# Kernel optimization log

Hardware: AMD Instinct MI355X
Metric: run time of the kernel (lower is better)

## Reference

```python
import jax, jax.numpy as jnp
import numpy as np

E, H, V, P, RAW = 512, 1024, 12000, 36, 2048
B, L = 128, 21

def setup_inputs() -> dict:
    key = jax.random.key(0)
    ks = jax.random.split(key, 16)
    n = lambda k, sh: (0.02 * jax.random.normal(k, sh)).astype(jnp.float32)
    z = lambda sh: jnp.zeros(sh, jnp.float32)
    return {
        "images_features": jax.random.normal(ks[0], (B, P, RAW), dtype=jnp.float32),
        "encoded_captions": jax.random.randint(ks[1], (B, L), 0, V),
        "caption_lengths": L,
        "W_img": n(ks[2], (RAW, H)), "b_img": z((H,)),
        "W_glob": n(ks[3], (H, E)), "b_glob": z((E,)),
        "W_ih1": n(ks[4], (2 * E + H, 4 * H)), "W_hh1": n(ks[5], (H, 4 * H)),
        "b_ih1": z((4 * H,)), "b_hh1": z((4 * H,)),
        "Wx_gate": n(ks[6], (2 * E + H, H)), "bx_gate": z((H,)),
        "Wh_gate": n(ks[7], (H, H)), "bh_gate": z((H,)),
        "W_ih2": n(ks[8], (2 * H, 4 * H)), "W_hh2": n(ks[9], (H, 4 * H)),
        "b_ih2": z((4 * H,)), "b_hh2": z((4 * H,)),
        "Wv": n(ks[10], (H, P)), "bv": z((P,)),
        "Ws": n(ks[11], (H, P)), "bs": z((P,)),
        "Wg": n(ks[12], (H, P)),
        "wh": n(ks[13], (P,)),
        "emb": n(ks[14], (V, E)),
        "W_fc": n(ks[15], (H, V)), "b_fc": z((V,)),
    }

def _lstm(x, h, c, W_ih, W_hh, b_ih, b_hh):
    # torch LSTMCell gate order: i, f, g, o
    g = x @ W_ih + b_ih + h @ W_hh + b_hh
    i, f, gg, o = jnp.split(g, 4, axis=-1)
    c_new = jax.nn.sigmoid(f) * c + jax.nn.sigmoid(i) * jnp.tanh(gg)
    h_new = jax.nn.sigmoid(o) * jnp.tanh(c_new)
    return h_new, c_new

def reference(images_features, encoded_captions, caption_lengths, W_img, b_img,
              W_glob, b_glob, W_ih1, W_hh1, b_ih1, b_hh1, Wx_gate, bx_gate,
              Wh_gate, bh_gate, W_ih2, W_hh2, b_ih2, b_hh2, Wv, bv, Ws, bs,
              Wg, wh, emb, W_fc, b_fc):
    Bsz = images_features.shape[0]
    Hd = W_hh1.shape[0]
    T = int(caption_lengths) - 1
    Vfeat = jax.nn.relu(images_features @ W_img + b_img)            # (B,P,H)
    glob = jax.nn.relu(jnp.mean(Vfeat, axis=1) @ W_glob + b_glob)   # (B,E)
    img_proj = Vfeat @ Wv + bv                                      # (B,P,P) loop-invariant
    word_embs = emb[encoded_captions[:, :T]]                        # (B,T,E)

    def step(carry, we):
        h1, c1, h2, c2 = carry
        xt = jnp.concatenate([h2, glob, we], axis=-1)               # (B, H+2E)
        h1n, c1n = _lstm(xt, h1, c1, W_ih1, W_hh1, b_ih1, b_hh1)
        sen_gate = jax.nn.sigmoid(xt @ Wx_gate + bx_gate + h1 @ Wh_gate + bh_gate)
        st = sen_gate * jnp.tanh(c1n)                               # visual sentinel
        ht_proj = h1n @ Wg                                          # (B,P)
        z = jnp.tanh(img_proj + ht_proj[:, :, None]) @ wh           # (B,P)
        alpha = jax.nn.softmax(z, axis=1)                           # (B,P)
        context = jnp.einsum('bp,bph->bh', alpha, Vfeat)            # (B,H)
        att_vs = jnp.tanh(st @ Ws + bs + ht_proj) @ wh              # (B,)
        alpha_hat = jax.nn.softmax(jnp.concatenate([z, att_vs[:, None]], axis=1), axis=1)
        beta = alpha_hat[:, -1:]                                    # (B,1)
        c_hat = beta * st + (1.0 - beta) * context
        h2n, c2n = _lstm(jnp.concatenate([c_hat, h1n], axis=-1), h2, c2,
                         W_ih2, W_hh2, b_ih2, b_hh2)
        score = (c_hat + h2n) @ W_fc + b_fc                         # (B,V)
        return (h1n, c1n, h2n, c2n), (score, alpha, beta)

    zeros = jnp.zeros((Bsz, Hd), images_features.dtype)
    init = (zeros, zeros, zeros, zeros)
    _, (preds, alphas, betas) = jax.lax.scan(step, init, jnp.swapaxes(word_embs, 0, 1))
    return (jnp.swapaxes(preds, 0, 1),   # (B,T,V)
            jnp.swapaxes(alphas, 0, 1),  # (B,T,P)
            jnp.swapaxes(betas, 0, 1))   # (B,T,1)
```

## Files before the change

### kernel.cpp

```cpp
#include <hip/hip_runtime.h>
#include <hip/hip_bf16.h>
#include <math.h>

typedef __attribute__((ext_vector_type(4))) float f32x4;
typedef __attribute__((ext_vector_type(8))) short bf16x8;

constexpr int kB = 128, kT = 20, kH = 1024, kE = 512, kP = 36, kRaw = 2048, kV = 12000;
constexpr int kSlab1 = kB * 5120;
constexpr int kSlab2 = kB * 4096;

__device__ __forceinline__ float sigf(float x) { return 1.0f / (1.0f + expf(-x)); }

#define AS1C const __attribute__((address_space(1))) void*
#define AS3P __attribute__((address_space(3))) void*

constexpr int NZ1 = 2 * kB * kH / 4;
constexpr int NZ2 = 2 * kB * kH * 2 / 16;
constexpr int NCV = kB * kP * kRaw / 4;
constexpr int NPV = 64 * 1024 * 2 / 16;
constexpr int NPF = 32 * 1024 * 2 / 16;
constexpr int NPB = 5120;
constexpr int NGE = kB * kT * kE;

__global__ __launch_bounds__(256) void prep_small(
    float* c1z, uint4* h1z, const float* images, __hip_bfloat16* imagesb,
    uint4* wtv, uint4* wtfc_pad,
    const float* b_ih1, const float* b_hh1, const float* bx, const float* bh,
    const float* b_ih2, const float* b_hh2, float* bias_g1, float* bias_g2,
    const int* caps, const float* emb, __hip_bfloat16* wembb) {
  long idx = (long)blockIdx.x * 256 + threadIdx.x;
  if (idx < NZ1) { reinterpret_cast<float4*>(c1z)[idx] = make_float4(0, 0, 0, 0); return; }
  idx -= NZ1;
  if (idx < NZ2) { h1z[idx] = make_uint4(0, 0, 0, 0); return; }
  idx -= NZ2;
  if (idx < NCV) {
    float4 v = reinterpret_cast<const float4*>(images)[idx];
    __hip_bfloat16* d = imagesb + idx * 4;
    d[0] = __float2bfloat16(v.x); d[1] = __float2bfloat16(v.y);
    d[2] = __float2bfloat16(v.z); d[3] = __float2bfloat16(v.w);
    return;
  }
  idx -= NCV;
  if (idx < NPV) { wtv[idx] = make_uint4(0, 0, 0, 0); return; }
  idx -= NPV;
  if (idx < NPF) { wtfc_pad[idx] = make_uint4(0, 0, 0, 0); return; }
  idx -= NPF;
  if (idx < NPB) {
    int i = (int)idx;
    if (i < 4096) {
      bias_g1[i] = b_ih1[i] + b_hh1[i];
      bias_g2[i] = b_ih2[i] + b_hh2[i];
    } else {
      bias_g1[i] = bx[i - 4096] + bh[i - 4096];
    }
    return;
  }
  idx -= NPB;
  if (idx < NGE) {
    int e = (int)(idx % kE);
    int bt = (int)(idx / kE);
    int t = bt % kT;
    int b = bt / kT;
    int tok = caps[b * (kT + 1) + t];
    wembb[idx] = __float2bfloat16(emb[(size_t)tok * kE + e]);
  }
}

struct TJob {
  const float* src; __hip_bfloat16* dst;
  int ld_src, K, N, lddst, koff, noff, blk_off, nbx;
};
struct TAll { TJob job[12]; int njobs; int total_blocks; };

__global__ __launch_bounds__(256) void transpose_all(TAll ta) {
  __shared__ float t[32][33];
  int bid = blockIdx.x;
  int ji = 0;
  while (ji + 1 < ta.njobs && bid >= ta.job[ji + 1].blk_off) ++ji;
  const TJob& J = ta.job[ji];
  int lbid = bid - J.blk_off;
  int n0 = (lbid % J.nbx) * 32, k0 = (lbid / J.nbx) * 32;
  int tx = threadIdx.x & 31, ty = threadIdx.x >> 5;
  #pragma unroll
  for (int i = 0; i < 32; i += 8) {
    int k = k0 + ty + i, n = n0 + tx;
    t[ty + i][tx] = (k < J.K && n < J.N) ? J.src[(size_t)k * J.ld_src + n] : 0.0f;
  }
  __syncthreads();
  #pragma unroll
  for (int i = 0; i < 32; i += 8) {
    int n = n0 + ty + i, k = k0 + tx;
    if (n < J.N && k < J.K)
      J.dst[(size_t)(n + J.noff) * J.lddst + k + J.koff] = __float2bfloat16(t[tx][ty + i]);
  }
}

struct SegB { const __hip_bfloat16* A; int lda; int kstart; int kend; };
struct GemmBArgs {
  SegB seg[4]; int nseg;
  const __hip_bfloat16* WT; int ldk;
  const float* bias;
  float* C; __hip_bfloat16* C16; int ldc; int N; int Ktot; int act; int zstride;
};

__global__ __launch_bounds__(256) void gemm_bf16(GemmBArgs ga) {
  __shared__ char lds[65536];
  const int bm = blockIdx.y * 64;
  const int bn = blockIdx.x * 64;
  const int tid = threadIdx.x;
  const int lane = tid & 63;
  const int w = tid >> 6;
  const int wr = w >> 1, wc = w & 1;

  int rowS[4], scbS[4], dstS[4];
  #pragma unroll
  for (int j = 0; j < 4; ++j) {
    int off = ((j * 4 + w) * 64 + lane) * 16;
    int row = off >> 8, colb = off & 255;
    rowS[j] = row;
    scbS[j] = colb ^ ((row & 7) << 4);
    dstS[j] = (j * 4 + w) * 1024;
  }

  f32x4 acc[2][2] = {};
  const int nz = gridDim.z;
  const int nit = (ga.Ktot >> 7) / nz;
  const int it0 = blockIdx.z * nit;
  float* C = ga.C + (size_t)blockIdx.z * ga.zstride;

  auto stage = [&](int it, int buf) {
    const int k0 = it << 7;
    int si = 0;
    while (k0 >= ga.seg[si].kend) ++si;
    const __hip_bfloat16* Aseg = ga.seg[si].A;
    const int lda = ga.seg[si].lda;
    const int ks = k0 - ga.seg[si].kstart;
    char* baseA = lds + buf * 32768;
    char* baseB = baseA + 16384;
    #pragma unroll
    for (int j = 0; j < 4; ++j) {
      const __hip_bfloat16* sA = Aseg + (size_t)(bm + rowS[j]) * lda + ks + (scbS[j] >> 1);
      __builtin_amdgcn_global_load_lds((AS1C)sA, (AS3P)(baseA + dstS[j]), 16, 0, 0);
      const __hip_bfloat16* sB = ga.WT + (size_t)(bn + rowS[j]) * ga.ldk + k0 + (scbS[j] >> 1);
      __builtin_amdgcn_global_load_lds((AS1C)sB, (AS3P)(baseB + dstS[j]), 16, 0, 0);
    }
  };

  auto compute = [&](int buf) {
    const char* baseA = lds + buf * 32768;
    const char* baseB = baseA + 16384;
    #pragma unroll
    for (int kk = 0; kk < 4; ++kk) {
      bf16x8 a[2], b[2];
      #pragma unroll
      for (int f = 0; f < 2; ++f) {
        int row = wr * 32 + f * 16 + (lane & 15);
        int cb = kk * 64 + (lane >> 4) * 16;
        a[f] = *(const bf16x8*)(baseA + row * 256 + (cb ^ ((row & 7) << 4)));
        int nl = wc * 32 + f * 16 + (lane & 15);
        b[f] = *(const bf16x8*)(baseB + nl * 256 + (cb ^ ((nl & 7) << 4)));
      }
      #pragma unroll
      for (int fm = 0; fm < 2; ++fm)
        #pragma unroll
        for (int fn = 0; fn < 2; ++fn)
          acc[fm][fn] = __builtin_amdgcn_mfma_f32_16x16x32_bf16(a[fm], b[fn], acc[fm][fn], 0, 0, 0);
    }
  };

  stage(it0, 0);
  stage(it0 + 1, 1);
  asm volatile("s_waitcnt vmcnt(8)" ::: "memory");
  __builtin_amdgcn_s_barrier();
  int cur = 0;
  for (int i = 0; i < nit; ++i) {
    compute(cur);
    __builtin_amdgcn_s_barrier();
    if (i + 2 < nit) stage(it0 + i + 2, cur);
    if (i + 1 < nit) {
      if (i + 2 < nit) asm volatile("s_waitcnt vmcnt(8)" ::: "memory");
      else             asm volatile("s_waitcnt vmcnt(0)" ::: "memory");
      __builtin_amdgcn_s_barrier();
    }
    cur ^= 1;
  }

  #pragma unroll
  for (int fm = 0; fm < 2; ++fm) {
    int rbase = bm + wr * 32 + fm * 16 + (lane >> 4) * 4;
    #pragma unroll
    for (int fn = 0; fn < 2; ++fn) {
      int col = bn + wc * 32 + fn * 16 + (lane & 15);
      if (col >= ga.N) continue;
      float bv = ga.bias ? ga.bias[col] : 0.0f;
      #pragma unroll
      for (int j = 0; j < 4; ++j) {
        float v = acc[fm][fn][j] + bv;
        if (ga.act == 1) v = fmaxf(v, 0.0f);
        size_t off = (size_t)(rbase + j) * ga.ldc + col;
        if (ga.C) C[off] = v;
        if (ga.C16) ga.C16[off] = __float2bfloat16(v);
      }
    }
  }
}

struct G128Args {
  const __hip_bfloat16* A; int lda;
  const __hip_bfloat16* WT; int ldk;
  const float* bias;
  float* C; __hip_bfloat16* C16; int ldc; int N; int Ktot; int act; int cmap; int morder;
};

template <int BK>
__global__ __launch_bounds__(256) void gemm128(G128Args ga) {
  constexpr int RB = BK * 2;
  constexpr int TILEB = 128 * RB;
  constexpr int ROUNDS = TILEB / 4096;
  constexpr int SWZ = (RB == 256) ? 15 : (RB == 128 ? 7 : 3);
  __shared__ char lds[2 * 2 * TILEB];
  const int gx = gridDim.x;
  const int gy = gridDim.y;
  const int nwg = gx * gy;
  int bid = blockIdx.y * gx + blockIdx.x;
  int q = nwg >> 3, r = nwg & 7;
  int xc = bid & 7, yq = bid >> 3;
  int swz = (xc < r ? xc * (q + 1) : r * (q + 1) + (xc - r) * q) + yq;
  int bn, bm;
  if (ga.morder == 1) { bm = (swz % gy) * 128; bn = (swz / gy) * 128; }
  else                { bn = (swz % gx) * 128; bm = (swz / gx) * 128; }

  const int tid = threadIdx.x;
  const int lane = tid & 63;
  const int w = tid >> 6;
  const int wr = w >> 1, wc = w & 1;

  int rowS[ROUNDS], scbS[ROUNDS], dstS[ROUNDS];
  #pragma unroll
  for (int j = 0; j < ROUNDS; ++j) {
    int off = ((j * 4 + w) * 64 + lane) * 16;
    int row = off / RB, colb = off % RB;
    rowS[j] = row;
    scbS[j] = colb ^ ((row & SWZ) << 4);
    dstS[j] = off;
  }

  f32x4 acc[4][4] = {};
  const int nit = ga.Ktot / BK;

  auto stage = [&](int it, int buf) {
    const int k0 = it * BK;
    char* baseA = lds + buf * 2 * TILEB;
    char* baseB = baseA + TILEB;
    #pragma unroll
    for (int j = 0; j < ROUNDS; ++j) {
      const __hip_bfloat16* sA = ga.A + (size_t)(bm + rowS[j]) * ga.lda + k0 + (scbS[j] >> 1);
      __builtin_amdgcn_global_load_lds((AS1C)sA, (AS3P)(baseA + dstS[j]), 16, 0, 0);
      const __hip_bfloat16* sB = ga.WT + (size_t)(bn + rowS[j]) * ga.ldk + k0 + (scbS[j] >> 1);
      __builtin_amdgcn_global_load_lds((AS1C)sB, (AS3P)(baseB + dstS[j]), 16, 0, 0);
    }
  };

  auto compute = [&](int buf) {
    const char* baseA = lds + buf * 2 * TILEB;
    const char* baseB = baseA + TILEB;
    #pragma unroll
    for (int kk = 0; kk < BK / 32; ++kk) {
      bf16x8 a[4], b[4];
      int cb = kk * 64 + (lane >> 4) * 16;
      #pragma unroll
      for (int f = 0; f < 4; ++f) {
        int row = wr * 64 + f * 16 + (lane & 15);
        a[f] = *(const bf16x8*)(baseA + row * RB + (cb ^ ((row & SWZ) << 4)));
        int nl = wc * 64 + f * 16 + (lane & 15);
        b[f] = *(const bf16x8*)(baseB + nl * RB + (cb ^ ((nl & SWZ) << 4)));
      }
      #pragma unroll
      for (int fm = 0; fm < 4; ++fm)
        #pragma unroll
        for (int fn = 0; fn < 4; ++fn)
          acc[fm][fn] = __builtin_amdgcn_mfma_f32_16x16x32_bf16(a[fm], b[fn], acc[fm][fn], 0, 0, 0);
    }
  };

  auto wait_one_stage = [&]() {
    if constexpr (ROUNDS == 4) asm volatile("s_waitcnt vmcnt(8)" ::: "memory");
    else                       asm volatile("s_waitcnt vmcnt(4)" ::: "memory");
  };

  stage(0, 0);
  stage(1, 1);
  wait_one_stage();
  __builtin_amdgcn_s_barrier();
  int cur = 0;
  for (int i = 0; i < nit; ++i) {
    compute(cur);
    __builtin_amdgcn_s_barrier();
    if (i + 2 < nit) stage(i + 2, cur);
    if (i + 1 < nit) {
      if (i + 2 < nit) wait_one_stage();
      else             asm volatile("s_waitcnt vmcnt(0)" ::: "memory");
      __builtin_amdgcn_s_barrier();
    }
    cur ^= 1;
  }

  #pragma unroll
  for (int fm = 0; fm < 4; ++fm) {
    int rbase = bm + wr * 64 + fm * 16 + (lane >> 4) * 4;
    #pragma unroll
    for (int fn = 0; fn < 4; ++fn) {
      int col = bn + wc * 64 + fn * 16 + (lane & 15);
      if (col >= ga.N) continue;
      float bv = ga.bias ? ga.bias[col] : 0.0f;
      #pragma unroll
      for (int j = 0; j < 4; ++j) {
        float v = acc[fm][fn][j] + bv;
        if (ga.act == 1) v = fmaxf(v, 0.0f);
        int m = rbase + j;
        size_t off = ga.cmap == 1
            ? (size_t)(m & 127) * ga.ldc + (size_t)(m >> 7) * kV + col
            : (size_t)m * ga.ldc + col;
        if (ga.C) ga.C[off] = v;
        if (ga.C16) ga.C16[off] = __float2bfloat16(v);
      }
    }
  }
}

__global__ __launch_bounds__(256) void mean_p(const float* __restrict__ Vfeat,
                                              __hip_bfloat16* __restrict__ meanVb) {
  int idx = blockIdx.x * 256 + threadIdx.x;
  if (idx >= kB * kH) return;
  int b = idx >> 10, h = idx & 1023;
  float sm = 0.0f;
  for (int p = 0; p < kP; ++p) sm += Vfeat[((size_t)b * kP + p) * kH + h];
  meanVb[idx] = __float2bfloat16(sm * (1.0f / kP));
}

__global__ __launch_bounds__(256) void step1_fused(
    const float* __restrict__ g, const float* __restrict__ bias_g1,
    float* __restrict__ c1, __hip_bfloat16* __restrict__ h1b,
    const float* __restrict__ img_proj, const float* __restrict__ Vfeat,
    const float* __restrict__ Wg, const float* __restrict__ Ws,
    const float* __restrict__ bs, const float* __restrict__ wh,
    float* __restrict__ c_hat, __hip_bfloat16* __restrict__ c_hatb,
    float* __restrict__ out_alphas, float* __restrict__ out_betas, int t) {
  const int b = blockIdx.x;
  const int tid = threadIdx.x;
  const int lane = tid & 63;
  const int w = tid >> 6;
  __shared__ float sh_h1[kH];
  __shared__ float sh_st[kH];
  __shared__ float wsum[4][36];
  __shared__ float htp[36];
  __shared__ float stp[36];
  __shared__ float alpha[kP];
  __shared__ float sred[4];

  const float* gr0 = g + (size_t)b * 5120;
  const float* gr1 = gr0 + kSlab1;
  const float* gr2 = gr1 + kSlab1;
  #pragma unroll
  for (int i = 0; i < 4; ++i) {
    int h = tid + i * 256;
    float ig = sigf(gr0[h]           + gr1[h]           + gr2[h]           + bias_g1[h]);
    float fg = sigf(gr0[kH + h]      + gr1[kH + h]      + gr2[kH + h]      + bias_g1[kH + h]);
    float gg = tanhf(gr0[2 * kH + h] + gr1[2 * kH + h]  + gr2[2 * kH + h]  + bias_g1[2 * kH + h]);
    float og = sigf(gr0[3 * kH + h]  + gr1[3 * kH + h]  + gr2[3 * kH + h]  + bias_g1[3 * kH + h]);
    int idx = b * kH + h;
    float c = fg * c1[idx] + ig * gg;
    float tc = tanhf(c);
    float hn = og * tc;
    c1[idx] = c;
    h1b[idx] = __float2bfloat16(hn);
    sh_h1[h] = hn;
    sh_st[h] = sigf(gr0[4 * kH + h] + gr1[4 * kH + h] + gr2[4 * kH + h] + bias_g1[4 * kH + h]) * tc;
  }
  __syncthreads();

  #pragma unroll
  for (int pass = 0; pass < 2; ++pass) {
    const float* vec = pass == 0 ? sh_h1 : sh_st;
    const float* W = pass == 0 ? Wg : Ws;
    float pg[36];
    #pragma unroll
    for (int j = 0; j < 36; ++j) pg[j] = 0.0f;
    #pragma unroll
    for (int i = 0; i < 4; ++i) {
      int hh = tid + i * 256;
      float hv = vec[hh];
      const float4* wrow = reinterpret_cast<const float4*>(W + (size_t)hh * 36);
      #pragma unroll
      for (int r = 0; r < 9; ++r) {
        float4 wv = wrow[r];
        pg[4 * r + 0] = fmaf(hv, wv.x, pg[4 * r + 0]);
        pg[4 * r + 1] = fmaf(hv, wv.y, pg[4 * r + 1]);
        pg[4 * r + 2] = fmaf(hv, wv.z, pg[4 * r + 2]);
        pg[4 * r + 3] = fmaf(hv, wv.w, pg[4 * r + 3]);
      }
    }
    #pragma unroll
    for (int j = 0; j < 36; ++j) {
      float v = pg[j];
      #pragma unroll
      for (int off = 32; off > 0; off >>= 1) v += __shfl_down(v, off, 64);
      if (lane == 0) wsum[w][j] = v;
    }
    __syncthreads();
    if (tid < 36) {
      float s = wsum[0][tid] + wsum[1][tid] + wsum[2][tid] + wsum[3][tid];
      if (pass == 0) htp[tid] = s; else stp[tid] = s;
    }
    __syncthreads();
  }

  if (w == 0) {
    float zz_r = -3.0e38f;
    if (lane < kP) {
      const float* ip = img_proj + ((size_t)b * kP + lane) * kP;
      float acc = 0.0f;
      #pragma unroll
      for (int j = 0; j < kP; ++j) acc = fmaf(tanhf(ip[j] + htp[j]), wh[j], acc);
      zz_r = acc;
    }
    float m = zz_r;
    #pragma unroll
    for (int off = 32; off > 0; off >>= 1) m = fmaxf(m, __shfl_xor(m, off, 64));
    float e = (lane < kP) ? expf(zz_r - m) : 0.0f;
    float s = e;
    #pragma unroll
    for (int off = 32; off > 0; off >>= 1) s += __shfl_xor(s, off, 64);
    if (lane < kP) alpha[lane] = e / s;
    if (lane == 0) { sred[2] = m; sred[3] = s; }
  } else if (w == 1) {
    float tv = 0.0f;
    if (lane < kP) tv = tanhf(stp[lane] + bs[lane] + htp[lane]) * wh[lane];
    #pragma unroll
    for (int off = 32; off > 0; off >>= 1) tv += __shfl_xor(tv, off, 64);
    if (lane == 0) sred[0] = tv;
  }
  __syncthreads();
  if (tid == 0) {
    float av = sred[0], m = sred[2], s = sred[3];
    float m2 = fmaxf(m, av);
    float eb = expf(av - m2);
    float beta = eb / (s * expf(m - m2) + eb);
    sred[1] = beta;
    out_betas[b * kT + t] = beta;
  }
  __syncthreads();
  if (tid < kP) out_alphas[((size_t)b * kT + t) * kP + tid] = alpha[tid];
  const float beta = sred[1];
  #pragma unroll
  for (int i = 0; i < 4; ++i) {
    int h = tid + i * 256;
    float ctx = 0.0f;
    for (int p = 0; p < kP; ++p) ctx = fmaf(alpha[p], Vfeat[((size_t)b * kP + p) * kH + h], ctx);
    float v = beta * sh_st[h] + (1.0f - beta) * ctx;
    c_hat[(size_t)b * kH + h] = v;
    c_hatb[(size_t)b * kH + h] = __float2bfloat16(v);
  }
}

__global__ __launch_bounds__(256) void lstm2_elem(const float* __restrict__ g,
                                                  const float* __restrict__ bias_g2,
                                                  float* __restrict__ c2,
                                                  __hip_bfloat16* __restrict__ h2b,
                                                  const float* __restrict__ c_hat,
                                                  __hip_bfloat16* __restrict__ sbufb) {
  int idx = blockIdx.x * 256 + threadIdx.x;
  if (idx >= kB * kH) return;
  int b = idx >> 10, h = idx & 1023;
  const float* gr0 = g + (size_t)b * 4 * kH;
  const float* gr1 = gr0 + kSlab2;
  const float* gr2 = gr1 + kSlab2;
  float ig = sigf(gr0[h]           + gr1[h]           + gr2[h]           + bias_g2[h]);
  float fg = sigf(gr0[kH + h]      + gr1[kH + h]      + gr2[kH + h]      + bias_g2[kH + h]);
  float gg = tanhf(gr0[2 * kH + h] + gr1[2 * kH + h]  + gr2[2 * kH + h]  + bias_g2[2 * kH + h]);
  float og = sigf(gr0[3 * kH + h]  + gr1[3 * kH + h]  + gr2[3 * kH + h]  + bias_g2[3 * kH + h]);
  float c = fg * c2[idx] + ig * gg;
  float hn = og * tanhf(c);
  c2[idx] = c;
  h2b[idx] = __float2bfloat16(hn);
  sbufb[idx] = __float2bfloat16(c_hat[idx] + hn);
}

extern "C" void kernel_launch(void* const* d_in, const int* in_sizes, int n_in,
                              void* d_out, int out_size, void* d_ws, size_t ws_size,
                              hipStream_t stream) {
  const float* images  = (const float*)d_in[0];
  const int*   caps    = (const int*)d_in[1];
  const float* W_img   = (const float*)d_in[3];
  const float* b_img   = (const float*)d_in[4];
  const float* W_glob  = (const float*)d_in[5];
  const float* b_glob  = (const float*)d_in[6];
  const float* W_ih1   = (const float*)d_in[7];
  const float* W_hh1   = (const float*)d_in[8];
  const float* b_ih1   = (const float*)d_in[9];
  const float* b_hh1   = (const float*)d_in[10];
  const float* Wx_gate = (const float*)d_in[11];
  const float* bx_gate = (const float*)d_in[12];
  const float* Wh_gate = (const float*)d_in[13];
  const float* bh_gate = (const float*)d_in[14];
  const float* W_ih2   = (const float*)d_in[15];
  const float* W_hh2   = (const float*)d_in[16];
  const float* b_ih2   = (const float*)d_in[17];
  const float* b_hh2   = (const float*)d_in[18];
  const float* Wv      = (const float*)d_in[19];
  const float* bv      = (const float*)d_in[20];
  const float* Ws_     = (const float*)d_in[21];
  const float* bs_     = (const float*)d_in[22];
  const float* Wg      = (const float*)d_in[23];
  const float* wh      = (const float*)d_in[24];
  const float* emb     = (const float*)d_in[25];
  const float* W_fc    = (const float*)d_in[26];
  const float* b_fc    = (const float*)d_in[27];

  float* out = (float*)d_out;
  float* out_alphas = out + (size_t)kB * kT * kV;
  float* out_betas  = out_alphas + (size_t)kB * kT * kP;

  char* base = (char*)d_ws;
  auto alloc = [&](size_t bytes) {
    char* p = base;
    base += (bytes + 255) & ~(size_t)255;
    return p;
  };
  float*          Vfeat   = (float*)alloc((size_t)kB * kP * kH * 4);
  __hip_bfloat16* Vfeatb  = (__hip_bfloat16*)alloc((size_t)kB * kP * kH * 2);
  __hip_bfloat16* imagesb = (__hip_bfloat16*)alloc((size_t)kB * kP * kRaw * 2);
  __hip_bfloat16* WTg1    = (__hip_bfloat16*)alloc((size_t)5120 * 3072 * 2);
  __hip_bfloat16* WTg2    = (__hip_bfloat16*)alloc((size_t)4096 * 3072 * 2);
  __hip_bfloat16* WTfc    = (__hip_bfloat16*)alloc((size_t)12032 * 1024 * 2);
  __hip_bfloat16* WTimg   = (__hip_bfloat16*)alloc((size_t)1024 * 2048 * 2);
  __hip_bfloat16* WTglob  = (__hip_bfloat16*)alloc((size_t)512 * 1024 * 2);
  __hip_bfloat16* WTv     = (__hip_bfloat16*)alloc((size_t)64 * 1024 * 2);
  __hip_bfloat16* wembb   = (__hip_bfloat16*)alloc((size_t)kB * kT * kE * 2);
  float*          img_proj= (float*)alloc((size_t)kB * kP * kP * 4);
  __hip_bfloat16* globb   = (__hip_bfloat16*)alloc((size_t)kB * kE * 2);
  __hip_bfloat16* meanVb  = (__hip_bfloat16*)alloc((size_t)kB * kH * 2);
  float*          c1      = (float*)alloc((size_t)2 * kB * kH * 4);
  float*          c2      = c1 + kB * kH;
  __hip_bfloat16* h1b     = (__hip_bfloat16*)alloc((size_t)2 * kB * kH * 2);
  __hip_bfloat16* h2b     = h1b + kB * kH;
  float*          g1out   = (float*)alloc((size_t)3 * kB * 5120 * 4);
  float*          chat    = (float*)alloc((size_t)kB * kH * 4);
  __hip_bfloat16* chatb   = (__hip_bfloat16*)alloc((size_t)kB * kH * 2);
  __hip_bfloat16* sbufall = (__hip_bfloat16*)alloc((size_t)kT * kB * kH * 2);
  float*          bias_g1 = (float*)alloc(5120 * 4);
  float*          bias_g2 = (float*)alloc(4096 * 4);

  {
    long total = (long)NZ1 + NZ2 + NCV + NPV + NPF + NPB + NGE;
    int blocks = (int)((total + 255) / 256);
    prep_small<<<blocks, 256, 0, stream>>>(
        c1, (uint4*)h1b, images, imagesb, (uint4*)WTv,
        (uint4*)(WTfc + (size_t)12000 * 1024),
        b_ih1, b_hh1, bx_gate, bh_gate, b_ih2, b_hh2, bias_g1, bias_g2,
        caps, emb, wembb);
  }
  {
    TAll ta = {};
    int off = 0, j = 0;
    auto add = [&](const float* src, int ldsrc, int K, int N, __hip_bfloat16* dst,
                   int lddst, int koff, int noff) {
      int nbx = (N + 31) / 32, nby = (K + 31) / 32;
      ta.job[j] = {src, dst, ldsrc, K, N, lddst, koff, noff, off, nbx};
      off += nbx * nby;
      ++j;
    };
    add(W_img,   kH,     kRaw, kH,     WTimg,  kRaw, 0, 0);
    add(W_glob,  kE,     kH,   kE,     WTglob, kH,   0, 0);
    add(Wv,      kP,     kH,   kP,     WTv,    kH,   0, 0);
    add(W_ih1,   4 * kH, 2048, 4 * kH, WTg1,   3072, 0, 0);
    add(W_hh1,   4 * kH, 1024, 4 * kH, WTg1,   3072, 2048, 0);
    add(Wx_gate, kH,     2048, kH,     WTg1,   3072, 0, 4096);
    add(Wh_gate, kH,     1024, kH,     WTg1,   3072, 2048, 4096);
    add(W_ih2,   4 * kH, 2048, 4 * kH, WTg2,   3072, 0, 0);
    add(W_hh2,   4 * kH, 1024, 4 * kH, WTg2,   3072, 2048, 0);
    add(W_fc,    kV,     kH,   kV,     WTfc,   kH,   0, 0);
    ta.njobs = j;
    ta.total_blocks = off;
    transpose_all<<<off, 256, 0, stream>>>(ta);
  }

  {
    G128Args ga = {};
    ga.A = imagesb; ga.lda = kRaw; ga.WT = WTimg; ga.ldk = kRaw; ga.bias = b_img;
    ga.C = Vfeat; ga.C16 = Vfeatb; ga.ldc = kH; ga.N = kH; ga.Ktot = kRaw;
    ga.act = 1; ga.cmap = 0; ga.morder = 0;
    gemm128<64><<<dim3(kH / 128, kB * kP / 128), 256, 0, stream>>>(ga);
  }
  mean_p<<<(kB * kH + 255) / 256, 256, 0, stream>>>(Vfeat, meanVb);
  {
    GemmBArgs ga = {};
    ga.seg[0] = {meanVb, kH, 0, kH};
    ga.nseg = 1; ga.WT = WTglob; ga.ldk = kH; ga.bias = b_glob;
    ga.C = nullptr; ga.C16 = globb; ga.ldc = kE; ga.N = kE; ga.Ktot = kH; ga.act = 1;
    gemm_bf16<<<dim3(kE / 64, kB / 64, 1), 256, 0, stream>>>(ga);
  }
  {
    GemmBArgs ga = {};
    ga.seg[0] = {Vfeatb, kH, 0, kH};
    ga.nseg = 1; ga.WT = WTv; ga.ldk = kH; ga.bias = bv;
    ga.C = img_proj; ga.C16 = nullptr; ga.ldc = kP; ga.N = kP; ga.Ktot = kH; ga.act = 0;
    gemm_bf16<<<dim3(1, kB * kP / 64, 1), 256, 0, stream>>>(ga);
  }

  for (int t = 0; t < kT; ++t) {
    {
      GemmBArgs ga = {};
      ga.seg[0] = {h2b, kH, 0, kH};
      ga.seg[1] = {globb, kE, kH, kH + kE};
      ga.seg[2] = {wembb + (size_t)t * kE, kT * kE, kH + kE, 2048};
      ga.seg[3] = {h1b, kH, 2048, 3072};
      ga.nseg = 4; ga.WT = WTg1; ga.ldk = 3072; ga.bias = nullptr;
      ga.C = g1out; ga.C16 = nullptr; ga.ldc = 5120; ga.N = 5120; ga.Ktot = 3072;
      ga.act = 0; ga.zstride = kSlab1;
      gemm_bf16<<<dim3(5120 / 64, kB / 64, 3), 256, 0, stream>>>(ga);
    }
    step1_fused<<<kB, 256, 0, stream>>>(g1out, bias_g1, c1, h1b, img_proj, Vfeat,
                                        Wg, Ws_, bs_, wh, chat, chatb,
                                        out_alphas, out_betas, t);
    {
      GemmBArgs ga = {};
      ga.seg[0] = {chatb, kH, 0, kH};
      ga.seg[1] = {h1b, kH, kH, 2048};
      ga.seg[2] = {h2b, kH, 2048, 3072};
      ga.nseg = 3; ga.WT = WTg2; ga.ldk = 3072; ga.bias = nullptr;
      ga.C = g1out; ga.C16 = nullptr; ga.ldc = 4096; ga.N = 4096; ga.Ktot = 3072;
      ga.act = 0; ga.zstride = kSlab2;
      gemm_bf16<<<dim3(4096 / 64, kB / 64, 3), 256, 0, stream>>>(ga);
    }
    lstm2_elem<<<(kB * kH + 255) / 256, 256, 0, stream>>>(
        g1out, bias_g2, c2, h2b, chat, sbufall + (size_t)t * kB * kH);
  }

  {
    G128Args ga = {};
    ga.A = sbufall; ga.lda = kH; ga.WT = WTfc; ga.ldk = kH; ga.bias = b_fc;
    ga.C = out; ga.C16 = nullptr; ga.ldc = kT * kV; ga.N = kV; ga.Ktot = kH;
    ga.act = 0; ga.cmap = 1; ga.morder = 1;
    gemm128<32><<<dim3(12032 / 128, kT * kB / 128), 256, 0, stream>>>(ga);
  }
}
```

Measured before the change: 1.537 ms.

## Fuse decode time loop into one persistent cooperative kernel with grid syncs

Replaces the 80 per-step kernel launches of the recurrent decode loop with a single cooperative kernel of 256 blocks. Inside it, the two gate GEMMs, the attention step and the LSTM2 elementwise update run in turn, separated by grid-wide barriers. The output-projection GEMM for step t-1 now runs on otherwise idle blocks during the attention phase of step t, instead of as one large GEMM at the end. The aim is to remove launch overhead and the tail idle time between kernels, and to hide the FC projection behind the serial recurrence. The cost is grid.sync overhead, uneven work per phase (480 tiles spread over 256 blocks), and smaller 64x64 tiles. A fallback to the old multi-kernel path runs if the cooperative launch fails. The LDS destination addressing in gemm128 is also changed to a wave-uniform base.

```diff
diff --git a/kernel.cpp b/kernel.cpp
--- a/kernel.cpp
+++ b/kernel.cpp
@@ -1,6 +1,9 @@
 #include <hip/hip_runtime.h>
+#include <hip/hip_cooperative_groups.h>
 #include <hip/hip_bf16.h>
 #include <math.h>
+
+namespace cg = cooperative_groups;
 
 typedef __attribute__((ext_vector_type(4))) float f32x4;
 typedef __attribute__((ext_vector_type(8))) short bf16x8;
@@ -242,7 +245,7 @@
     int row = off / RB, colb = off % RB;
     rowS[j] = row;
     scbS[j] = colb ^ ((row & SWZ) << 4);
-    dstS[j] = off;
+    dstS[j] = (j * 4 + w) * 1024;
   }
 
   f32x4 acc[4][4] = {};
@@ -484,6 +487,374 @@
   c2[idx] = c;
   h2b[idx] = __float2bfloat16(hn);
   sbufb[idx] = __float2bfloat16(c_hat[idx] + hn);
+}
+
+struct LoopArgs {
+  const __hip_bfloat16 *WTg1, *WTg2, *WTfc;
+  const __hip_bfloat16 *globb, *wembb;
+  __hip_bfloat16 *h1b, *h2b, *chatb;
+  float *g1out, *c1, *c2, *chat;
+  const float *bias_g1, *bias_g2, *b_fc;
+  const float *img_proj, *Vfeat;
+  const float *Wg, *Ws, *bs, *wh;
+  float *out, *out_alphas, *out_betas;
+  __hip_bfloat16 *sbufall;
+};
+
+__device__ void gemm64_tile(char* lds, const SegB* seg, const __hip_bfloat16* WT,
+                            int ldk, int bm, int bn, int it0, int nit,
+                            float* C, int ldc) {
+  const int tid = threadIdx.x;
+  const int lane = tid & 63;
+  const int w = tid >> 6;
+  const int wr = w >> 1, wc = w & 1;
+  __syncthreads();
+
+  int rowS[4], scbS[4], dstS[4];
+  #pragma unroll
+  for (int j = 0; j < 4; ++j) {
+    int off = ((j * 4 + w) * 64 + lane) * 16;
+    int row = off >> 8, colb = off & 255;
+    rowS[j] = row;
+    scbS[j] = colb ^ ((row & 7) << 4);
+    dstS[j] = (j * 4 + w) * 1024;
+  }
+
+  f32x4 acc[2][2] = {};
+
+  auto stage = [&](int it, int buf) {
+    const int k0 = it << 7;
+    int si = 0;
+    while (k0 >= seg[si].kend) ++si;
+    const __hip_bfloat16* Aseg = seg[si].A;
+    const int lda = seg[si].lda;
+    const int ks = k0 - seg[si].kstart;
+    char* baseA = lds + buf * 32768;
+    char* baseB = baseA + 16384;
+    #pragma unroll
+    for (int j = 0; j < 4; ++j) {
+      const __hip_bfloat16* sA = Aseg + (size_t)(bm + rowS[j]) * lda + ks + (scbS[j] >> 1);
+      __builtin_amdgcn_global_load_lds((AS1C)sA, (AS3P)(baseA + dstS[j]), 16, 0, 0);
+      const __hip_bfloat16* sB = WT + (size_t)(bn + rowS[j]) * ldk + k0 + (scbS[j] >> 1);
+      __builtin_amdgcn_global_load_lds((AS1C)sB, (AS3P)(baseB + dstS[j]), 16, 0, 0);
+    }
+  };
+  auto compute = [&](int buf) {
+    const char* baseA = lds + buf * 32768;
+    const char* baseB = baseA + 16384;
+    #pragma unroll
+    for (int kk = 0; kk < 4; ++kk) {
+      bf16x8 a[2], b[2];
+      #pragma unroll
+      for (int f = 0; f < 2; ++f) {
+        int row = wr * 32 + f * 16 + (lane & 15);
+        int cb = kk * 64 + (lane >> 4) * 16;
+        a[f] = *(const bf16x8*)(baseA + row * 256 + (cb ^ ((row & 7) << 4)));
+        int nl = wc * 32 + f * 16 + (lane & 15);
+        b[f] = *(const bf16x8*)(baseB + nl * 256 + (cb ^ ((nl & 7) << 4)));
+      }
+      #pragma unroll
+      for (int fm = 0; fm < 2; ++fm)
+        #pragma unroll
+        for (int fn = 0; fn < 2; ++fn)
+          acc[fm][fn] = __builtin_amdgcn_mfma_f32_16x16x32_bf16(a[fm], b[fn], acc[fm][fn], 0, 0, 0);
+    }
+  };
+
+  stage(it0, 0);
+  stage(it0 + 1, 1);
+  asm volatile("s_waitcnt vmcnt(8)" ::: "memory");
+  __builtin_amdgcn_s_barrier();
+  int cur = 0;
+  for (int i = 0; i < nit; ++i) {
+    compute(cur);
+    __builtin_amdgcn_s_barrier();
+    if (i + 2 < nit) stage(it0 + i + 2, cur);
+    if (i + 1 < nit) {
+      if (i + 2 < nit) asm volatile("s_waitcnt vmcnt(8)" ::: "memory");
+      else             asm volatile("s_waitcnt vmcnt(0)" ::: "memory");
+      __builtin_amdgcn_s_barrier();
+    }
+    cur ^= 1;
+  }
+
+  #pragma unroll
+  for (int fm = 0; fm < 2; ++fm) {
+    int rbase = bm + wr * 32 + fm * 16 + (lane >> 4) * 4;
+    #pragma unroll
+    for (int fn = 0; fn < 2; ++fn) {
+      int col = bn + wc * 32 + fn * 16 + (lane & 15);
+      #pragma unroll
+      for (int j = 0; j < 4; ++j)
+        C[(size_t)(rbase + j) * ldc + col] = acc[fm][fn][j];
+    }
+  }
+}
+
+__device__ void fc_tile(char* lds, const LoopArgs& A, int t, int bn) {
+  const int tid = threadIdx.x;
+  const int lane = tid & 63;
+  const int w = tid >> 6;
+  const int wr = w >> 1, wc = w & 1;
+  const int bm = t * 128;
+  __syncthreads();
+
+  int rowS[4], scbS[4], dstS[4];
+  #pragma unroll
+  for (int j = 0; j < 4; ++j) {
+    int off = ((j * 4 + w) * 64 + lane) * 16;
+    int row = off >> 7, colb = off & 127;
+    rowS[j] = row;
+    scbS[j] = colb ^ ((row & 7) << 4);
+    dstS[j] = (j * 4 + w) * 1024;
+  }
+
+  f32x4 acc[4][4] = {};
+  const int nit = 16;
+
+  auto stage = [&](int it, int buf) {
+    const int k0 = it << 6;
+    char* baseA = lds + buf * 32768;
+    char* baseB = baseA + 16384;
+    #pragma unroll
+    for (int j = 0; j < 4; ++j) {
+      const __hip_bfloat16* sA = A.sbufall + (size_t)(bm + rowS[j]) * kH + k0 + (scbS[j] >> 1);
+      __builtin_amdgcn_global_load_lds((AS1C)sA, (AS3P)(baseA + dstS[j]), 16, 0, 0);
+      const __hip_bfloat16* sB = A.WTfc + (size_t)(bn + rowS[j]) * kH + k0 + (scbS[j] >> 1);
+      __builtin_amdgcn_global_load_lds((AS1C)sB, (AS3P)(baseB + dstS[j]), 16, 0, 0);
+    }
+  };
+  auto compute = [&](int buf) {
+    const char* baseA = lds + buf * 32768;
+    const char* baseB = baseA + 16384;
+    #pragma unroll
+    for (int kk = 0; kk < 2; ++kk) {
+      bf16x8 a[4], b[4];
+      int cb = kk * 64 + (lane >> 4) * 16;
+      #pragma unroll
+      for (int f = 0; f < 4; ++f) {
+        int row = wr * 64 + f * 16 + (lane & 15);
+        a[f] = *(const bf16x8*)(baseA + row * 128 + (cb ^ ((row & 7) << 4)));
+        int nl = wc * 64 + f * 16 + (lane & 15);
+        b[f] = *(const bf16x8*)(baseB + nl * 128 + (cb ^ ((nl & 7) << 4)));
+      }
+      #pragma unroll
+      for (int fm = 0; fm < 4; ++fm)
+        #pragma unroll
+        for (int fn = 0; fn < 4; ++fn)
+          acc[fm][fn] = __builtin_amdgcn_mfma_f32_16x16x32_bf16(a[fm], b[fn], acc[fm][fn], 0, 0, 0);
+    }
+  };
+
+  stage(0, 0);
+  stage(1, 1);
+  asm volatile("s_waitcnt vmcnt(8)" ::: "memory");
+  __builtin_amdgcn_s_barrier();
+  int cur = 0;
+  for (int i = 0; i < nit; ++i) {
+    compute(cur);
+    __builtin_amdgcn_s_barrier();
+    if (i + 2 < nit) stage(i + 2, cur);
+    if (i + 1 < nit) {
+      if (i + 2 < nit) asm volatile("s_waitcnt vmcnt(8)" ::: "memory");
+      else             asm volatile("s_waitcnt vmcnt(0)" ::: "memory");
+      __builtin_amdgcn_s_barrier();
+    }
+    cur ^= 1;
+  }
+
+  #pragma unroll
+  for (int fm = 0; fm < 4; ++fm) {
+    int rbase = wr * 64 + fm * 16 + (lane >> 4) * 4;
+    #pragma unroll
+    for (int fn = 0; fn < 4; ++fn) {
+      int col = bn + wc * 64 + fn * 16 + (lane & 15);
+      if (col >= kV) continue;
+      float bv = A.b_fc[col];
+      #pragma unroll
+      for (int j = 0; j < 4; ++j) {
+        int b = rbase + j;
+        A.out[(size_t)b * (kT * kV) + (size_t)t * kV + col] = acc[fm][fn][j] + bv;
+      }
+    }
+  }
+}
+
+__device__ void step1_dev(char* ldsc, const LoopArgs& A, int b, int t) {
+  const int tid = threadIdx.x;
+  const int lane = tid & 63;
+  const int w = tid >> 6;
+  float* S = (float*)ldsc;
+  float* sh_h1 = S;
+  float* sh_st = S + 1024;
+  float* wsum  = S + 2048;
+  float* htp   = S + 2192;
+  float* stp   = S + 2228;
+  float* alpha = S + 2264;
+  float* sred  = S + 2300;
+  __syncthreads();
+
+  const float* gr0 = A.g1out + (size_t)b * 5120;
+  const float* gr1 = gr0 + kSlab1;
+  const float* gr2 = gr1 + kSlab1;
+  #pragma unroll
+  for (int i = 0; i < 4; ++i) {
+    int h = tid + i * 256;
+    float ig = sigf(gr0[h]           + gr1[h]           + gr2[h]           + A.bias_g1[h]);
+    float fg = sigf(gr0[kH + h]      + gr1[kH + h]      + gr2[kH + h]      + A.bias_g1[kH + h]);
+    float gg = tanhf(gr0[2 * kH + h] + gr1[2 * kH + h]  + gr2[2 * kH + h]  + A.bias_g1[2 * kH + h]);
+    float og = sigf(gr0[3 * kH + h]  + gr1[3 * kH + h]  + gr2[3 * kH + h]  + A.bias_g1[3 * kH + h]);
+    int idx = b * kH + h;
+    float c = fg * A.c1[idx] + ig * gg;
+    float tc = tanhf(c);
+    float hn = og * tc;
+    A.c1[idx] = c;
+    A.h1b[idx] = __float2bfloat16(hn);
+    sh_h1[h] = hn;
+    sh_st[h] = sigf(gr0[4 * kH + h] + gr1[4 * kH + h] + gr2[4 * kH + h] + A.bias_g1[4 * kH + h]) * tc;
+  }
+  __syncthreads();
+
+  #pragma unroll
+  for (int pass = 0; pass < 2; ++pass) {
+    const float* vec = pass == 0 ? sh_h1 : sh_st;
+    const float* W = pass == 0 ? A.Wg : A.Ws;
+    float pg[36];
+    #pragma unroll
+    for (int j = 0; j < 36; ++j) pg[j] = 0.0f;
+    #pragma unroll
+    for (int i = 0; i < 4; ++i) {
+      int hh = tid + i * 256;
+      float hv = vec[hh];
+      const float4* wrow = reinterpret_cast<const float4*>(W + (size_t)hh * 36);
+      #pragma unroll
+      for (int r = 0; r < 9; ++r) {
+        float4 wv = wrow[r];
+        pg[4 * r + 0] = fmaf(hv, wv.x, pg[4 * r + 0]);
+        pg[4 * r + 1] = fmaf(hv, wv.y, pg[4 * r + 1]);
+        pg[4 * r + 2] = fmaf(hv, wv.z, pg[4 * r + 2]);
+        pg[4 * r + 3] = fmaf(hv, wv.w, pg[4 * r + 3]);
+      }
+    }
+    #pragma unroll
+    for (int j = 0; j < 36; ++j) {
+      float v = pg[j];
+      #pragma unroll
+      for (int off = 32; off > 0; off >>= 1) v += __shfl_down(v, off, 64);
+      if (lane == 0) wsum[w * 36 + j] = v;
+    }
+    __syncthreads();
+    if (tid < 36) {
+      float s = wsum[tid] + wsum[36 + tid] + wsum[72 + tid] + wsum[108 + tid];
+      if (pass == 0) htp[tid] = s; else stp[tid] = s;
+    }
+    __syncthreads();
+  }
+
+  if (w == 0) {
+    float zz_r = -3.0e38f;
+    if (lane < kP) {
+      const float* ip = A.img_proj + ((size_t)b * kP + lane) * kP;
+      float acc = 0.0f;
+      #pragma unroll
+      for (int j = 0; j < kP; ++j) acc = fmaf(tanhf(ip[j] + htp[j]), A.wh[j], acc);
+      zz_r = acc;
+    }
+    float m = zz_r;
+    #pragma unroll
+    for (int off = 32; off > 0; off >>= 1) m = fmaxf(m, __shfl_xor(m, off, 64));
+    float e = (lane < kP) ? expf(zz_r - m) : 0.0f;
+    float s = e;
+    #pragma unroll
+    for (int off = 32; off > 0; off >>= 1) s += __shfl_xor(s, off, 64);
+    if (lane < kP) alpha[lane] = e / s;
+    if (lane == 0) { sred[2] = m; sred[3] = s; }
+  } else if (w == 1) {
+    float tv = 0.0f;
+    if (lane < kP) tv = tanhf(stp[lane] + A.bs[lane] + htp[lane]) * A.wh[lane];
+    #pragma unroll
+    for (int off = 32; off > 0; off >>= 1) tv += __shfl_xor(tv, off, 64);
+    if (lane == 0) sred[0] = tv;
+  }
+  __syncthreads();
+  if (tid == 0) {
+    float av = sred[0], m = sred[2], s = sred[3];
+    float m2 = fmaxf(m, av);
+    float eb = expf(av - m2);
+    float beta = eb / (s * expf(m - m2) + eb);
+    sred[1] = beta;
+    A.out_betas[b * kT + t] = beta;
+  }
+  __syncthreads();
+  if (tid < kP) A.out_alphas[((size_t)b * kT + t) * kP + tid] = alpha[tid];
+  const float beta = sred[1];
+  #pragma unroll
+  for (int i = 0; i < 4; ++i) {
+    int h = tid + i * 256;
+    float ctx = 0.0f;
+    for (int p = 0; p < kP; ++p)
+      ctx = fmaf(alpha[p], A.Vfeat[((size_t)b * kP + p) * kH + h], ctx);
+    float v = beta * sh_st[h] + (1.0f - beta) * ctx;
+    A.chat[(size_t)b * kH + h] = v;
+    A.chatb[(size_t)b * kH + h] = __float2bfloat16(v);
+  }
+}
+
+__device__ void lstm2_one(const LoopArgs& A, int idx, int t) {
+  int b = idx >> 10, h = idx & 1023;
+  const float* gr0 = A.g1out + (size_t)b * 4 * kH;
+  const float* gr1 = gr0 + kSlab2;
+  float ig = sigf(gr0[h]           + gr1[h]           + A.bias_g2[h]);
+  float fg = sigf(gr0[kH + h]      + gr1[kH + h]      + A.bias_g2[kH + h]);
+  float gg = tanhf(gr0[2 * kH + h] + gr1[2 * kH + h]  + A.bias_g2[2 * kH + h]);
+  float og = sigf(gr0[3 * kH + h]  + gr1[3 * kH + h]  + A.bias_g2[3 * kH + h]);
+  float c = fg * A.c2[idx] + ig * gg;
+  float hn = og * tanhf(c);
+  A.c2[idx] = c;
+  A.h2b[idx] = __float2bfloat16(hn);
+  A.sbufall[(size_t)t * kB * kH + idx] = __float2bfloat16(A.chat[idx] + hn);
+}
+
+__global__ __launch_bounds__(256) void decode_loop(LoopArgs A) {
+  __shared__ char lds[65536];
+  cg::grid_group grid = cg::this_grid();
+  const int bid = blockIdx.x;
+
+  for (int t = 0; t < kT; ++t) {
+    {
+      SegB seg[4] = {{A.h2b, kH, 0, kH},
+                     {A.globb, kE, kH, kH + kE},
+                     {A.wembb + (size_t)t * kE, kT * kE, kH + kE, 2048},
+                     {A.h1b, kH, 2048, 3072}};
+      for (int item = bid; item < 480; item += 256) {
+        int z = item / 160, rem = item % 160;
+        int bm = (rem / 80) * 64, bn = (rem % 80) * 64;
+        gemm64_tile(lds, seg, A.WTg1, 3072, bm, bn, z * 8, 8,
+                    A.g1out + (size_t)z * kSlab1, 5120);
+      }
+    }
+    grid.sync();
+    if (bid < 128) {
+      step1_dev(lds, A, bid, t);
+    } else if (t > 0 && bid - 128 < 94) {
+      fc_tile(lds, A, t - 1, (bid - 128) * 128);
+    }
+    grid.sync();
+    {
+      SegB seg[3] = {{A.chatb, kH, 0, kH},
+                     {A.h1b, kH, kH, 2048},
+                     {A.h2b, kH, 2048, 3072}};
+      int z = bid / 128, rem = bid % 128;
+      int bm = (rem / 64) * 64, bn = (rem % 64) * 64;
+      gemm64_tile(lds, seg, A.WTg2, 3072, bm, bn, z * 12, 12,
+                  A.g1out + (size_t)z * kSlab2, 4096);
+    }
+    grid.sync();
+    lstm2_one(A, bid * 512 + threadIdx.x, t);
+    lstm2_one(A, bid * 512 + 256 + threadIdx.x, t);
+    grid.sync();
+  }
+  if (bid < 94) fc_tile(lds, A, kT - 1, bid * 128);
 }
 
 extern "C" void kernel_launch(void* const* d_in, const int* in_sizes, int n_in,
@@ -608,36 +979,49 @@
     gemm_bf16<<<dim3(1, kB * kP / 64, 1), 256, 0, stream>>>(ga);
   }
 
-  for (int t = 0; t < kT; ++t) {
-    {
-      GemmBArgs ga = {};
-      ga.seg[0] = {h2b, kH, 0, kH};
-      ga.seg[1] = {globb, kE, kH, kH + kE};
-      ga.seg[2] = {wembb + (size_t)t * kE, kT * kE, kH + kE, 2048};
-      ga.seg[3] = {h1b, kH, 2048, 3072};
-      ga.nseg = 4; ga.WT = WTg1; ga.ldk = 3072; ga.bias = nullptr;
-      ga.C = g1out; ga.C16 = nullptr; ga.ldc = 5120; ga.N = 5120; ga.Ktot = 3072;
-      ga.act = 0; ga.zstride = kSlab1;
-      gemm_bf16<<<dim3(5120 / 64, kB / 64, 3), 256, 0, stream>>>(ga);
-    }
-    step1_fused<<<kB, 256, 0, stream>>>(g1out, bias_g1, c1, h1b, img_proj, Vfeat,
-                                        Wg, Ws_, bs_, wh, chat, chatb,
-                                        out_alphas, out_betas, t);
-    {
-      GemmBArgs ga = {};
-      ga.seg[0] = {chatb, kH, 0, kH};
-      ga.seg[1] = {h1b, kH, kH, 2048};
-      ga.seg[2] = {h2b, kH, 2048, 3072};
-      ga.nseg = 3; ga.WT = WTg2; ga.ldk = 3072; ga.bias = nullptr;
-      ga.C = g1out; ga.C16 = nullptr; ga.ldc = 4096; ga.N = 4096; ga.Ktot = 3072;
-      ga.act = 0; ga.zstride = kSlab2;
-      gemm_bf16<<<dim3(4096 / 64, kB / 64, 3), 256, 0, stream>>>(ga);
-    }
-    lstm2_elem<<<(kB * kH + 255) / 256, 256, 0, stream>>>(
-        g1out, bias_g2, c2, h2b, chat, sbufall + (size_t)t * kB * kH);
-  }
-
-  {
+  LoopArgs la = {};
+  la.WTg1 = WTg1; la.WTg2 = WTg2; la.WTfc = WTfc;
+  la.globb = globb; la.wembb = wembb;
+  la.h1b = h1b; la.h2b = h2b; la.chatb = chatb;
+  la.g1out = g1out; la.c1 = c1; la.c2 = c2; la.chat = chat;
+  la.bias_g1 = bias_g1; la.bias_g2 = bias_g2; la.b_fc = b_fc;
+  la.img_proj = img_proj; la.Vfeat = Vfeat;
+  la.Wg = Wg; la.Ws = Ws_; la.bs = bs_; la.wh = wh;
+  la.out = out; la.out_alphas = out_alphas; la.out_betas = out_betas;
+  la.sbufall = sbufall;
+  void* kargs[] = {(void*)&la};
+  hipError_t cerr = hipLaunchCooperativeKernel(decode_loop, dim3(256), dim3(256),
+                                               kargs, 0u, stream);
+  if (cerr != hipSuccess) {
+    (void)hipGetLastError();
+    for (int t = 0; t < kT; ++t) {
+      {
+        GemmBArgs ga = {};
+        ga.seg[0] = {h2b, kH, 0, kH};
+        ga.seg[1] = {globb, kE, kH, kH + kE};
+        ga.seg[2] = {wembb + (size_t)t * kE, kT * kE, kH + kE, 2048};
+        ga.seg[3] = {h1b, kH, 2048, 3072};
+        ga.nseg = 4; ga.WT = WTg1; ga.ldk = 3072; ga.bias = nullptr;
+        ga.C = g1out; ga.C16 = nullptr; ga.ldc = 5120; ga.N = 5120; ga.Ktot = 3072;
+        ga.act = 0; ga.zstride = kSlab1;
+        gemm_bf16<<<dim3(5120 / 64, kB / 64, 3), 256, 0, stream>>>(ga);
+      }
+      step1_fused<<<kB, 256, 0, stream>>>(g1out, bias_g1, c1, h1b, img_proj, Vfeat,
+                                          Wg, Ws_, bs_, wh, chat, chatb,
+                                          out_alphas, out_betas, t);
+      {
+        GemmBArgs ga = {};
+        ga.seg[0] = {chatb, kH, 0, kH};
+        ga.seg[1] = {h1b, kH, kH, 2048};
+        ga.seg[2] = {h2b, kH, 2048, 3072};
+        ga.nseg = 3; ga.WT = WTg2; ga.ldk = 3072; ga.bias = nullptr;
+        ga.C = g1out; ga.C16 = nullptr; ga.ldc = 4096; ga.N = 4096; ga.Ktot = 3072;
+        ga.act = 0; ga.zstride = kSlab2;
+        gemm_bf16<<<dim3(4096 / 64, kB / 64, 3), 256, 0, stream>>>(ga);
+      }
+      lstm2_elem<<<(kB * kH + 255) / 256, 256, 0, stream>>>(
+          g1out, bias_g2, c2, h2b, chat, sbufall + (size_t)t * kB * kH);
+    }
     G128Args ga = {};
     ga.A = sbufall; ga.lda = kH; ga.WT = WTfc; ga.ldk = kH; ga.bias = b_fc;
     ga.C = out; ga.C16 = nullptr; ga.ldc = kT * kV; ga.N = kV; ga.Ktot = kH;
```

Result: slower. 5.661 ms (+268.2%).
